# Optimization experiments

Measured on AMD Instinct MI355X. Metric: run time of the kernel, lower is better.

## Reference

```python
import jax, jax.numpy as jnp
import numpy as np

LN_EPS = 1e-5

def _ln(x, g, b):
    m = x.mean(-1, keepdims=True)
    v = ((x - m) ** 2).mean(-1, keepdims=True)
    return (x - m) * jax.lax.rsqrt(v + LN_EPS) * g + b

def setup_inputs() -> dict:
    key = jax.random.key(0)
    B, Q, K, H, NH, L = 4, 32, 8192, 1024, 16, 128
    ks = jax.random.split(key, 10)
    def p(k, shape):
        return jax.random.normal(k, shape, jnp.float32) * 0.02
    return {
        "question_emb": jax.random.normal(ks[0], (B, Q, H), jnp.float32),
        "context_emb": jax.random.normal(ks[1], (B, K, H), jnp.float32),
        "Wq_l": p(ks[2], (H, H)), "bq_l": jnp.zeros((H,), jnp.float32),
        "Wk_l": p(ks[3], (H, H)), "bk_l": jnp.zeros((H,), jnp.float32),
        "Wq_g": p(ks[4], (H, H)), "bq_g": jnp.zeros((H,), jnp.float32),
        "Wk_g": p(ks[5], (H, H)), "bk_g": jnp.zeros((H,), jnp.float32),
        "ln_g": jnp.ones((H,), jnp.float32), "ln_b": jnp.zeros((H,), jnp.float32),
        "gp_W1": p(ks[6], (2 * H, H)), "gp_b1": jnp.zeros((H,), jnp.float32),
        "gp_W2": p(ks[7], (H, 1)), "gp_b2": jnp.zeros((1,), jnp.float32),
        "num_heads": NH,
        "chunk_len": L,
    }

def reference(question_emb, context_emb, Wq_l, bq_l, Wk_l, bk_l,
              Wq_g, bq_g, Wk_g, bk_g, ln_g, ln_b,
              gp_W1, gp_b1, gp_W2, gp_b2, num_heads, chunk_len):
    B, Qn, H = question_emb.shape
    K = context_emb.shape[1]
    nh, L = num_heads, chunk_len
    d = H // nh
    J = K // L
    scale = 1.0 / np.sqrt(d)

    # ---- Global scorer: one cross-attn over all K, then per-chunk mean pooling ----
    qh = (question_emb @ Wq_g + bq_g).reshape(B, Qn, nh, d).transpose(0, 2, 1, 3)   # [B,nh,Q,d]
    kh = (context_emb @ Wk_g + bk_g).reshape(B, K, nh, d).transpose(0, 2, 1, 3)     # [B,nh,K,d]
    wg = jax.nn.softmax(jnp.einsum('bhqd,bhkd->bhqk', qh, kh) * scale, axis=-1)     # [B,nh,Q,K]
    attn = wg.mean(axis=(1, 2))                                                     # [B,K]
    global_scores = jax.nn.softmax(attn.reshape(B, J, L).mean(-1), axis=-1)         # [B,J]

    # ---- Local scorer: per-chunk cross-attn (batched over chunks), max-over-keys pooling ----
    qh_l = (question_emb @ Wq_l + bq_l).reshape(B, Qn, nh, d).transpose(0, 2, 1, 3)  # [B,nh,Q,d]
    kh_l = (context_emb @ Wk_l + bk_l).reshape(B, J, L, nh, d).transpose(0, 1, 3, 2, 4)  # [B,J,nh,L,d]
    s_l = jnp.einsum('bhqd,bjhld->bjhql', qh_l, kh_l) * scale                        # [B,J,nh,Q,L]
    w_l = jax.nn.softmax(s_l, axis=-1)
    local_scores = jax.nn.softmax(w_l.max(-1).mean(axis=(2, 3)), axis=-1)            # [B,J]

    # ---- Router: LN'd mean-pool vecs -> gate MLP -> fuse -> softmax ----
    q_vec = _ln(question_emb.mean(1), ln_g, ln_b)                                    # [B,H]
    c_vec = _ln(context_emb.reshape(B, J, L, H).mean(2), ln_g, ln_b)                 # [B,J,H]
    g_in = jnp.concatenate([jnp.broadcast_to(q_vec[:, None, :], (B, J, H)), c_vec], -1)
    h1 = jax.nn.gelu(g_in @ gp_W1 + gp_b1, approximate=False)
    gate = jax.nn.sigmoid(h1 @ gp_W2 + gp_b2)[..., 0]                                # [B,J]
    fused = gate * local_scores + (1.0 - gate) * global_scores
    final_scores = jax.nn.softmax(fused, axis=-1)                                    # [B,J]
    global_gate = final_scores.mean(-1).reshape(B, 1, 1)
    return final_scores, local_scores, global_scores, global_gate
```

## Files before the change

### kernel.cpp

```cpp
#include <hip/hip_runtime.h>
#include <math.h>

#define B_    4
#define QN    32
#define KN    8192
#define HDIM  1024
#define NHD   16
#define DH    64
#define LCH   128
#define JCH   64

typedef float f32x4 __attribute__((ext_vector_type(4)));
typedef short s16x8 __attribute__((ext_vector_type(8)));
typedef unsigned short u16;

__device__ __forceinline__ u16 f2bf(float f) {
  unsigned u = __float_as_uint(f);
  u += 0x7fffu + ((u >> 16) & 1u);
  return (u16)(u >> 16);
}

__device__ __forceinline__ void llds16(const void* g, void* l) {
  __builtin_amdgcn_global_load_lds((const __attribute__((address_space(1))) unsigned int*)g,
                                   (__attribute__((address_space(3))) unsigned int*)l,
                                   16, 0, 0);
}

__device__ __forceinline__ void gemm64_direct(const float* __restrict__ A, const float* __restrict__ Bm,
                                              float* __restrict__ C, int m0, int n0, char* smem) {
  float (*As)[17] = (float(*)[17])smem;
  float (*Bs)[64] = (float(*)[64])(smem + 4352);
  int t = threadIdx.x;
  int tm = t >> 4, tn = t & 15;
  int ra = t >> 2, ka = (t & 3) * 4;
  int kb = t >> 4, nb = (t & 15) * 4;
  float c[4][4];
#pragma unroll
  for (int i = 0; i < 4; ++i)
#pragma unroll
    for (int j = 0; j < 4; ++j) c[i][j] = 0.f;
  for (int kk = 0; kk < HDIM; kk += 16) {
    float4 va = *(const float4*)(A + (size_t)(m0 + ra) * HDIM + kk + ka);
    float4 vb = *(const float4*)(Bm + (size_t)(kk + kb) * HDIM + n0 + nb);
    As[ra][ka] = va.x; As[ra][ka + 1] = va.y; As[ra][ka + 2] = va.z; As[ra][ka + 3] = va.w;
    *(float4*)&Bs[kb][nb] = vb;
    __syncthreads();
#pragma unroll
    for (int kq = 0; kq < 16; ++kq) {
      float a0 = As[tm * 4 + 0][kq], a1 = As[tm * 4 + 1][kq];
      float a2 = As[tm * 4 + 2][kq], a3 = As[tm * 4 + 3][kq];
      float b0 = Bs[kq][tn * 4 + 0], b1 = Bs[kq][tn * 4 + 1];
      float b2 = Bs[kq][tn * 4 + 2], b3 = Bs[kq][tn * 4 + 3];
      c[0][0] += a0 * b0; c[0][1] += a0 * b1; c[0][2] += a0 * b2; c[0][3] += a0 * b3;
      c[1][0] += a1 * b0; c[1][1] += a1 * b1; c[1][2] += a1 * b2; c[1][3] += a1 * b3;
      c[2][0] += a2 * b0; c[2][1] += a2 * b1; c[2][2] += a2 * b2; c[2][3] += a2 * b3;
      c[3][0] += a3 * b0; c[3][1] += a3 * b1; c[3][2] += a3 * b2; c[3][3] += a3 * b3;
    }
    __syncthreads();
  }
#pragma unroll
  for (int i = 0; i < 4; ++i)
#pragma unroll
    for (int j = 0; j < 4; ++j)
      C[(size_t)(m0 + tm * 4 + i) * HDIM + n0 + tn * 4 + j] = c[i][j];
}

__global__ __launch_bounds__(256) void k_phaseA(const float* __restrict__ ctx, u16* __restrict__ ctxb,
                                                const float* __restrict__ g, const float* __restrict__ lb,
                                                float* __restrict__ cvec,
                                                const float* __restrict__ question,
                                                const float* __restrict__ Wq_g, const float* __restrict__ Wq_l,
                                                float* __restrict__ qh, float* __restrict__ qvec,
                                                float* __restrict__ qpart) {
  __shared__ __align__(16) char smem[8448];
  int blk = blockIdx.x, t = threadIdx.x;
  if (blk < 256) {
    int bj = blk;
    const float* p = ctx + (size_t)bj * LCH * HDIM + t * 4;
    u16* op = ctxb + (size_t)bj * LCH * HDIM + t * 4;
    float a0 = 0, a1 = 0, a2 = 0, a3 = 0;
    for (int r = 0; r < LCH; ++r) {
      float4 v = *(const float4*)(p + (size_t)r * HDIM);
      ushort4 o;
      o.x = f2bf(v.x); o.y = f2bf(v.y); o.z = f2bf(v.z); o.w = f2bf(v.w);
      *(ushort4*)(op + (size_t)r * HDIM) = o;
      a0 += v.x; a1 += v.y; a2 += v.z; a3 += v.w;
    }
    const float sc = 1.0f / LCH;
    a0 *= sc; a1 *= sc; a2 *= sc; a3 *= sc;
    float s = a0 + a1 + a2 + a3;
    float ss = a0 * a0 + a1 * a1 + a2 * a2 + a3 * a3;
#pragma unroll
    for (int o = 1; o < 64; o <<= 1) { s += __shfl_xor(s, o, 64); ss += __shfl_xor(ss, o, 64); }
    float* sm = (float*)smem; float* sq = sm + 4;
    int wid = t >> 6, lane = t & 63;
    if (lane == 0) { sm[wid] = s; sq[wid] = ss; }
    __syncthreads();
    float S = sm[0] + sm[1] + sm[2] + sm[3], SS = sq[0] + sq[1] + sq[2] + sq[3];
    float mu = S / HDIM;
    float inv = rsqrtf(SS / HDIM - mu * mu + 1e-5f);
    int c = t * 4;
    float4 o;
    o.x = (a0 - mu) * inv * g[c + 0] + lb[c + 0];
    o.y = (a1 - mu) * inv * g[c + 1] + lb[c + 1];
    o.z = (a2 - mu) * inv * g[c + 2] + lb[c + 2];
    o.w = (a3 - mu) * inv * g[c + 3] + lb[c + 3];
    *(float4*)&cvec[(size_t)bj * HDIM + c] = o;
  } else if (blk < 320) {
    int id = blk - 256;
    int s2 = id >> 5, mt = (id >> 4) & 1, ntile = id & 15;
    gemm64_direct(question, s2 ? Wq_l : Wq_g, qh + (size_t)s2 * 131072, mt * 64, ntile * 64, smem);
  } else if (blk < 324) {
    int b = blk - 320;
    const float* p = question + (size_t)b * QN * HDIM + t * 4;
    float a0 = 0, a1 = 0, a2 = 0, a3 = 0;
    for (int r = 0; r < QN; ++r) {
      float4 v = *(const float4*)(p + (size_t)r * HDIM);
      a0 += v.x; a1 += v.y; a2 += v.z; a3 += v.w;
    }
    const float sc = 1.0f / QN;
    a0 *= sc; a1 *= sc; a2 *= sc; a3 *= sc;
    float s = a0 + a1 + a2 + a3;
    float ss = a0 * a0 + a1 * a1 + a2 * a2 + a3 * a3;
#pragma unroll
    for (int o = 1; o < 64; o <<= 1) { s += __shfl_xor(s, o, 64); ss += __shfl_xor(ss, o, 64); }
    float* sm = (float*)smem; float* sq = sm + 4;
    int wid = t >> 6, lane = t & 63;
    if (lane == 0) { sm[wid] = s; sq[wid] = ss; }
    __syncthreads();
    float S = sm[0] + sm[1] + sm[2] + sm[3], SS = sq[0] + sq[1] + sq[2] + sq[3];
    float mu = S / HDIM;
    float inv = rsqrtf(SS / HDIM - mu * mu + 1e-5f);
    int c = t * 4;
    float4 o;
    o.x = (a0 - mu) * inv * g[c + 0] + lb[c + 0];
    o.y = (a1 - mu) * inv * g[c + 1] + lb[c + 1];
    o.z = (a2 - mu) * inv * g[c + 2] + lb[c + 2];
    o.w = (a3 - mu) * inv * g[c + 3] + lb[c + 3];
    *(float4*)&qvec[(size_t)b * HDIM + c] = o;
  } else {
    float4 z = make_float4(0.f, 0.f, 0.f, 0.f);
#pragma unroll
    for (int i = 0; i < 4; ++i) ((float4*)qpart)[t * 4 + i] = z;
  }
}

__global__ __launch_bounds__(256) void k_phaseB(const float* __restrict__ qh,
                                                const float* __restrict__ Wk_g, const float* __restrict__ Wk_l,
                                                const float* __restrict__ bq_g, const float* __restrict__ bq_l,
                                                u16* __restrict__ Ab,
                                                const float* __restrict__ bk_g, const float* __restrict__ bk_l,
                                                float* __restrict__ sbias,
                                                const float* __restrict__ qvec, const float* __restrict__ W1,
                                                float* __restrict__ qpart,
                                                const float* __restrict__ cvec, float* __restrict__ h1) {
  __shared__ __align__(16) char smem[8448];
  int blk = blockIdx.x, t = threadIdx.x;
  if (blk < 512) {
    int ct = blk & 3, slot = (blk >> 2) & 31, b = blk >> 7;
    int s2 = slot >> 4, h = slot & 15;
    const float* qhp = qh + (size_t)(s2 * 4 + b) * QN * HDIM;
    const float* Wk = s2 ? Wk_l : Wk_g;
    const float* bq = s2 ? bq_l : bq_g;
    float (*qs)[DH] = (float(*)[DH])smem;
    {
      int q = t >> 3, doff = (t & 7) * 8;
      const float4* src = (const float4*)(qhp + (size_t)q * HDIM + h * DH + doff);
      float4 b0 = *(const float4*)(bq + h * DH + doff);
      float4 b1 = *(const float4*)(bq + h * DH + doff + 4);
      float4 v0 = src[0], v1 = src[1];
      qs[q][doff + 0] = v0.x + b0.x; qs[q][doff + 1] = v0.y + b0.y;
      qs[q][doff + 2] = v0.z + b0.z; qs[q][doff + 3] = v0.w + b0.w;
      qs[q][doff + 4] = v1.x + b1.x; qs[q][doff + 5] = v1.y + b1.y;
      qs[q][doff + 6] = v1.z + b1.z; qs[q][doff + 7] = v1.w + b1.w;
    }
    __syncthreads();
    int c = ct * 256 + t;
    float w[DH];
    const float* wr = Wk + (size_t)c * HDIM + h * DH;
#pragma unroll
    for (int d = 0; d < DH; d += 4) {
      float4 v = *(const float4*)(wr + d);
      w[d] = v.x; w[d + 1] = v.y; w[d + 2] = v.z; w[d + 3] = v.w;
    }
    u16* outp = Ab + ((size_t)b * HDIM + s2 * 512 + h * QN) * HDIM + c;
    for (int q = 0; q < QN; ++q) {
      float acc = 0.f;
#pragma unroll
      for (int d = 0; d < DH; ++d) acc += qs[q][d] * w[d];
      outp[(size_t)q * HDIM] = f2bf(acc * 0.125f);
    }
  } else if (blk < 528) {
    int i = (blk - 512) * 256 + t;
    int b = i >> 10, n = i & (HDIM - 1);
    int s2 = n >> 9, hq = n & 511, h = hq >> 5, q = hq & 31;
    const float* qr = qh + ((size_t)(s2 * 4 + b) * QN + q) * HDIM + h * DH;
    const float* bk = (s2 ? bk_l : bk_g) + h * DH;
    const float* bq = (s2 ? bq_l : bq_g) + h * DH;
    float acc = 0.f;
#pragma unroll
    for (int d = 0; d < DH; ++d) acc += (qr[d] + bq[d]) * bk[d];
    sbias[i] = acc * 0.125f;
  } else if (blk < 784) {
    int id = blk - 528;
    int nt = id & 3, b = (id >> 2) & 3, ks = id >> 4;
    int n = nt * 256 + t;
    const float* qv = qvec + (size_t)b * HDIM + ks * 64;
    const float* wp = W1 + (size_t)ks * 64 * HDIM + n;
    float acc = 0.f;
#pragma unroll 8
    for (int c = 0; c < 64; ++c) acc += qv[c] * wp[(size_t)c * HDIM];
    atomicAdd(&qpart[(size_t)b * HDIM + n], acc);
  } else {
    int id = blk - 784;
    int mt = id >> 4, ntile = id & 15;
    gemm64_direct(cvec, W1 + 1048576, h1, mt * 64, ntile * 64, smem);
  }
}

__global__ __launch_bounds__(512, 2) void k_scores(const u16* __restrict__ ctxb, const u16* __restrict__ Ab,
                                                   const float* __restrict__ sbias,
                                                   float* __restrict__ mglob, float* __restrict__ zglob,
                                                   float* __restrict__ locinv) {
  __shared__ u16 lds[65536];
  u16* A0 = lds;           u16* B0 = lds + 16384;
  u16* A1 = lds + 32768;   u16* B1 = lds + 49152;
  int bid = blockIdx.x;
  int work = (bid & 7) * 64 + (bid >> 3);
  int b = work >> 7, rem = work & 127, rt = rem >> 2, nt = rem & 3;
  int t = threadIdx.x, wid = t >> 6, lane = t & 63;
  int wm = wid >> 2, wn = wid & 3;
  int lrow = lane & 15, lkg = lane >> 4;

  const u16* ctx0 = ctxb + ((size_t)b * KN + rt * 256) * HDIM;
  const u16* Afp  = Ab + ((size_t)b * HDIM + nt * 256) * HDIM;

  int grow = wid * 8 + (lane >> 3);
  int gslot = (lane & 7) ^ (lane >> 3);
  const u16* gA[4]; const u16* gB[4]; int dof[4];
#pragma unroll
  for (int s = 0; s < 4; ++s) {
    gA[s] = ctx0 + (size_t)(s * 64 + grow) * HDIM + gslot * 8;
    gB[s] = Afp + (size_t)(s * 64 + grow) * HDIM + gslot * 8;
    dof[s] = s * 4096 + wid * 512;
  }

  int rowA = (wm * 128 + lrow) * 64;
  int rowB = (wn * 64 + lrow) * 64;
  int p8[2];
#pragma unroll
  for (int ks = 0; ks < 2; ++ks) p8[ks] = ((ks * 4 + lkg) ^ (lane & 7)) * 8;

  f32x4 acc[8][4];
#pragma unroll
  for (int mi = 0; mi < 8; ++mi)
#pragma unroll
    for (int ni = 0; ni < 4; ++ni) acc[mi][ni] = 0.f;

#define STAGE(AT, BT, KT) { \
  _Pragma("unroll") for (int s = 0; s < 4; ++s) { \
    llds16(gA[s] + (KT) * 64, (AT) + dof[s]); \
    llds16(gB[s] + (KT) * 64, (BT) + dof[s]); } }

#define COMPUTE(AT, BT) { \
  _Pragma("unroll") for (int ks = 0; ks < 2; ++ks) { \
    const u16* pA = (AT) + rowA + p8[ks]; \
    const u16* pB = (BT) + rowB + p8[ks]; \
    s16x8 av[8], bv[4]; \
    _Pragma("unroll") for (int mi = 0; mi < 8; ++mi) av[mi] = *(const s16x8*)(pA + mi * 1024); \
    _Pragma("unroll") for (int ni = 0; ni < 4; ++ni) bv[ni] = *(const s16x8*)(pB + ni * 1024); \
    _Pragma("unroll") for (int mi = 0; mi < 8; ++mi) \
    _Pragma("unroll") for (int ni = 0; ni < 4; ++ni) \
      acc[mi][ni] = __builtin_amdgcn_mfma_f32_16x16x32_bf16(av[mi], bv[ni], acc[mi][ni], 0, 0, 0); } }

#define SYNCN(N) { asm volatile("s_waitcnt vmcnt(" #N ")" ::: "memory"); \
                   __builtin_amdgcn_s_barrier(); \
                   __builtin_amdgcn_sched_barrier(0); }

#define SUB(KT, CA, CB, SA, SB, FULL) { \
  if (FULL) { STAGE(SA, SB, (KT) + 1); } \
  if (FULL) { SYNCN(8) } else { SYNCN(0) } \
  __builtin_amdgcn_s_setprio(1); \
  COMPUTE(CA, CB); \
  __builtin_amdgcn_s_setprio(0); \
  __builtin_amdgcn_s_barrier(); }

  STAGE(A0, B0, 0);
  SUB(0,  A0, B0, A1, B1, 1)
  SUB(1,  A1, B1, A0, B0, 1)
  SUB(2,  A0, B0, A1, B1, 1)
  SUB(3,  A1, B1, A0, B0, 1)
  SUB(4,  A0, B0, A1, B1, 1)
  SUB(5,  A1, B1, A0, B0, 1)
  SUB(6,  A0, B0, A1, B1, 1)
  SUB(7,  A1, B1, A0, B0, 1)
  SUB(8,  A0, B0, A1, B1, 1)
  SUB(9,  A1, B1, A0, B0, 1)
  SUB(10, A0, B0, A1, B1, 1)
  SUB(11, A1, B1, A0, B0, 1)
  SUB(12, A0, B0, A1, B1, 1)
  SUB(13, A1, B1, A0, B0, 1)
  SUB(14, A0, B0, A1, B1, 1)
  SUB(15, A1, B1, A0, B0, 0)
#undef STAGE
#undef COMPUTE
#undef SYNCN
#undef SUB

  int jc = rt * 2 + wm;
  float sb[4];
#pragma unroll
  for (int ni = 0; ni < 4; ++ni)
    sb[ni] = sbias[b * HDIM + nt * 256 + wn * 64 + ni * 16 + lrow];
#pragma unroll
  for (int ni = 0; ni < 4; ++ni) {
    float m = -1e30f;
#pragma unroll
    for (int mi = 0; mi < 8; ++mi)
#pragma unroll
      for (int r = 0; r < 4; ++r) m = fmaxf(m, acc[mi][ni][r]);
    m += sb[ni];
    m = fmaxf(m, __shfl_xor(m, 16, 64));
    m = fmaxf(m, __shfl_xor(m, 32, 64));
    float z = 0.f;
#pragma unroll
    for (int mi = 0; mi < 8; ++mi)
#pragma unroll
      for (int r = 0; r < 4; ++r) z += __expf(acc[mi][ni][r] + sb[ni] - m);
    z += __shfl_xor(z, 16, 64);
    z += __shfl_xor(z, 32, 64);
    if (lane < 16) {
      int n = nt * 256 + wn * 64 + ni * 16 + lane;
      if (n < 512) {
        size_t o = ((size_t)b * 512 + n) * JCH + jc;
        mglob[o] = m; zglob[o] = z;
      } else {
        locinv[((size_t)b * JCH + jc) * 512 + (n - 512)] = 1.0f / z;
      }
    }
  }
}

__global__ __launch_bounds__(256) void k_hq(const float* __restrict__ mglob, const float* __restrict__ zglob,
                                            float* __restrict__ Mh, float* __restrict__ Zr) {
  int id = blockIdx.x * 256 + threadIdx.x;
  int b = id >> 9, hq = id & 511;
  const float* mg = mglob + ((size_t)b * 512 + hq) * JCH;
  const float* zg = zglob + ((size_t)b * 512 + hq) * JCH;
  float m = -1e30f;
  for (int j = 0; j < JCH; ++j) m = fmaxf(m, mg[j]);
  float z = 0.f;
  for (int j = 0; j < JCH; ++j) z += zg[j] * __expf(mg[j] - m);
  Mh[id] = m;
  Zr[id] = 1.0f / z;
}

__global__ __launch_bounds__(256) void k_chunk(const float* __restrict__ mglob, const float* __restrict__ zglob,
                                               const float* __restrict__ locinv,
                                               const float* __restrict__ Mh, const float* __restrict__ Zr,
                                               const float* __restrict__ h1, const float* __restrict__ qpart,
                                               const float* __restrict__ b1, const float* __restrict__ W2,
                                               float* __restrict__ abuf, float* __restrict__ lbuf,
                                               float* __restrict__ gbuf) {
  int bj = blockIdx.x, t = threadIdx.x;
  int b = bj >> 6, j = bj & 63;
  const float* mg = mglob + (size_t)b * 512 * JCH + j;
  const float* zg = zglob + (size_t)b * 512 * JCH + j;
  const float* lp = locinv + (size_t)bj * 512;
  const float* Mb = Mh + (size_t)b * 512;
  const float* Zb = Zr + (size_t)b * 512;
  float a = 0.f, l = 0.f, gsum = 0.f;
  for (int hq = t; hq < 512; hq += 256) {
    a += zg[(size_t)hq * JCH] * __expf(mg[(size_t)hq * JCH] - Mb[hq]) * Zb[hq];
    l += lp[hq];
  }
  const float* hp = h1 + (size_t)bj * HDIM;
  const float* qp = qpart + (size_t)b * HDIM;
  for (int n = t; n < HDIM; n += 256) {
    float x = hp[n] + qp[n] + b1[n];
    x = x * 0.5f * (1.0f + erff(x * 0.70710678118654752f));
    gsum += x * W2[n];
  }
#pragma unroll
  for (int o = 1; o < 64; o <<= 1) {
    a += __shfl_xor(a, o, 64); l += __shfl_xor(l, o, 64); gsum += __shfl_xor(gsum, o, 64);
  }
  __shared__ float ra[4], rl[4], rg[4];
  int wid = t >> 6, lane = t & 63;
  if (lane == 0) { ra[wid] = a; rl[wid] = l; rg[wid] = gsum; }
  __syncthreads();
  if (t == 0) {
    abuf[bj] = (ra[0] + ra[1] + ra[2] + ra[3]) * (1.0f / 65536.0f);
    lbuf[bj] = (rl[0] + rl[1] + rl[2] + rl[3]) * (1.0f / 512.0f);
    gbuf[bj] = rg[0] + rg[1] + rg[2] + rg[3];
  }
}

__global__ __launch_bounds__(64) void k_final(const float* __restrict__ abuf, const float* __restrict__ lbuf,
                                              const float* __restrict__ gbuf, const float* __restrict__ b2,
                                              float* __restrict__ out) {
  int b = blockIdx.x, t = threadIdx.x;
  float a = abuf[b * 64 + t];
  float l = lbuf[b * 64 + t];
  float gt = gbuf[b * 64 + t] + b2[0];
  gt = 1.0f / (1.0f + __expf(-gt));
  float am = a, lm = l;
#pragma unroll
  for (int o = 1; o < 64; o <<= 1) { am = fmaxf(am, __shfl_xor(am, o, 64)); lm = fmaxf(lm, __shfl_xor(lm, o, 64)); }
  float ae = __expf(a - am), le = __expf(l - lm);
  float as_ = ae, ls_ = le;
#pragma unroll
  for (int o = 1; o < 64; o <<= 1) { as_ += __shfl_xor(as_, o, 64); ls_ += __shfl_xor(ls_, o, 64); }
  float gs = ae / as_, ls = le / ls_;
  float fu = gt * ls + (1.0f - gt) * gs;
  float fm = fu;
#pragma unroll
  for (int o = 1; o < 64; o <<= 1) fm = fmaxf(fm, __shfl_xor(fm, o, 64));
  float fe = __expf(fu - fm);
  float fs_ = fe;
#pragma unroll
  for (int o = 1; o < 64; o <<= 1) fs_ += __shfl_xor(fs_, o, 64);
  float fv = fe / fs_;
  out[b * 64 + t] = fv;
  out[256 + b * 64 + t] = ls;
  out[512 + b * 64 + t] = gs;
  float tot = fv;
#pragma unroll
  for (int o = 1; o < 64; o <<= 1) tot += __shfl_xor(tot, o, 64);
  if (t == 0) out[768 + b] = tot * (1.0f / 64.0f);
}

extern "C" void kernel_launch(void* const* d_in, const int* in_sizes, int n_in,
                              void* d_out, int out_size, void* d_ws, size_t ws_size,
                              hipStream_t stream) {
  const float* question = (const float*)d_in[0];
  const float* context  = (const float*)d_in[1];
  const float* Wq_l = (const float*)d_in[2];
  const float* bq_l = (const float*)d_in[3];
  const float* Wk_l = (const float*)d_in[4];
  const float* bk_l = (const float*)d_in[5];
  const float* Wq_g = (const float*)d_in[6];
  const float* bq_g = (const float*)d_in[7];
  const float* Wk_g = (const float*)d_in[8];
  const float* bk_g = (const float*)d_in[9];
  const float* ln_g = (const float*)d_in[10];
  const float* ln_b = (const float*)d_in[11];
  const float* W1   = (const float*)d_in[12];
  const float* b1   = (const float*)d_in[13];
  const float* W2   = (const float*)d_in[14];
  const float* b2   = (const float*)d_in[15];

  char* ws = (char*)d_ws;
  u16*   ctxb   = (u16*)(ws + 0);
  u16*   Ab     = (u16*)(ws + 67108864);
  float* qh     = (float*)(ws + 75497472);
  float* sbias  = (float*)(ws + 76546048);
  float* mglob  = (float*)(ws + 76562432);
  float* zglob  = (float*)(ws + 77086720);
  float* locinv = (float*)(ws + 77611008);
  float* qvec   = (float*)(ws + 78135296);
  float* cvec   = (float*)(ws + 78151680);
  float* qpart  = (float*)(ws + 79200256);
  float* h1     = (float*)(ws + 79216640);
  float* Mh     = (float*)(ws + 80265216);
  float* Zr     = (float*)(ws + 80273408);
  float* abuf   = (float*)(ws + 80281600);
  float* lbuf   = (float*)(ws + 80282624);
  float* gbuf   = (float*)(ws + 80283648);

  hipLaunchKernelGGL(k_phaseA, dim3(325), dim3(256), 0, stream,
                     context, ctxb, ln_g, ln_b, cvec, question, Wq_g, Wq_l, qh, qvec, qpart);
  hipLaunchKernelGGL(k_phaseB, dim3(848), dim3(256), 0, stream,
                     qh, Wk_g, Wk_l, bq_g, bq_l, Ab, bk_g, bk_l, sbias, qvec, W1, qpart, cvec, h1);
  hipLaunchKernelGGL(k_scores, dim3(512), dim3(512), 0, stream, ctxb, Ab, sbias, mglob, zglob, locinv);
  hipLaunchKernelGGL(k_hq, dim3(8), dim3(256), 0, stream, mglob, zglob, Mh, Zr);
  hipLaunchKernelGGL(k_chunk, dim3(256), dim3(256), 0, stream, mglob, zglob, locinv, Mh, Zr, h1, qpart, b1, W2, abuf, lbuf, gbuf);
  hipLaunchKernelGGL(k_final, dim3(4), dim3(64), 0, stream, abuf, lbuf, gbuf, b2, (float*)d_out);
}
```

Before: 230.4 us.

## Split context conversion across row segments and defer LN/gate GEMM to later kernels

Result: slower. 245.8 us (+6.7%).

```diff
diff --git a/kernel.cpp b/kernel.cpp
--- a/kernel.cpp
+++ b/kernel.cpp
@@ -65,53 +65,36 @@
       C[(size_t)(m0 + tm * 4 + i) * HDIM + n0 + tn * 4 + j] = c[i][j];
 }
 
-__global__ __launch_bounds__(256) void k_phaseA(const float* __restrict__ ctx, u16* __restrict__ ctxb,
-                                                const float* __restrict__ g, const float* __restrict__ lb,
-                                                float* __restrict__ cvec,
-                                                const float* __restrict__ question,
-                                                const float* __restrict__ Wq_g, const float* __restrict__ Wq_l,
-                                                float* __restrict__ qh, float* __restrict__ qvec,
-                                                float* __restrict__ qpart) {
+__global__ __launch_bounds__(256) void k_cvt(const float* __restrict__ ctx, u16* __restrict__ ctxb,
+                                             float* __restrict__ csum4,
+                                             const float* __restrict__ question,
+                                             const float* __restrict__ Wq_g, const float* __restrict__ Wq_l,
+                                             float* __restrict__ qh,
+                                             const float* __restrict__ g, const float* __restrict__ lb,
+                                             float* __restrict__ qvec, float* __restrict__ qpart) {
   __shared__ __align__(16) char smem[8448];
   int blk = blockIdx.x, t = threadIdx.x;
-  if (blk < 256) {
-    int bj = blk;
-    const float* p = ctx + (size_t)bj * LCH * HDIM + t * 4;
-    u16* op = ctxb + (size_t)bj * LCH * HDIM + t * 4;
+  if (blk < 1024) {
+    int bj = blk >> 2, seg = blk & 3;
+    const float* p = ctx + ((size_t)bj * LCH + seg * 32) * HDIM + t * 4;
+    u16* op = ctxb + ((size_t)bj * LCH + seg * 32) * HDIM + t * 4;
     float a0 = 0, a1 = 0, a2 = 0, a3 = 0;
-    for (int r = 0; r < LCH; ++r) {
+#pragma unroll 8
+    for (int r = 0; r < 32; ++r) {
       float4 v = *(const float4*)(p + (size_t)r * HDIM);
       ushort4 o;
       o.x = f2bf(v.x); o.y = f2bf(v.y); o.z = f2bf(v.z); o.w = f2bf(v.w);
       *(ushort4*)(op + (size_t)r * HDIM) = o;
       a0 += v.x; a1 += v.y; a2 += v.z; a3 += v.w;
     }
-    const float sc = 1.0f / LCH;
-    a0 *= sc; a1 *= sc; a2 *= sc; a3 *= sc;
-    float s = a0 + a1 + a2 + a3;
-    float ss = a0 * a0 + a1 * a1 + a2 * a2 + a3 * a3;
-#pragma unroll
-    for (int o = 1; o < 64; o <<= 1) { s += __shfl_xor(s, o, 64); ss += __shfl_xor(ss, o, 64); }
-    float* sm = (float*)smem; float* sq = sm + 4;
-    int wid = t >> 6, lane = t & 63;
-    if (lane == 0) { sm[wid] = s; sq[wid] = ss; }
-    __syncthreads();
-    float S = sm[0] + sm[1] + sm[2] + sm[3], SS = sq[0] + sq[1] + sq[2] + sq[3];
-    float mu = S / HDIM;
-    float inv = rsqrtf(SS / HDIM - mu * mu + 1e-5f);
-    int c = t * 4;
-    float4 o;
-    o.x = (a0 - mu) * inv * g[c + 0] + lb[c + 0];
-    o.y = (a1 - mu) * inv * g[c + 1] + lb[c + 1];
-    o.z = (a2 - mu) * inv * g[c + 2] + lb[c + 2];
-    o.w = (a3 - mu) * inv * g[c + 3] + lb[c + 3];
-    *(float4*)&cvec[(size_t)bj * HDIM + c] = o;
-  } else if (blk < 320) {
-    int id = blk - 256;
+    float4 s4 = make_float4(a0, a1, a2, a3);
+    *(float4*)&csum4[((size_t)bj * 4 + seg) * HDIM + t * 4] = s4;
+  } else if (blk < 1088) {
+    int id = blk - 1024;
     int s2 = id >> 5, mt = (id >> 4) & 1, ntile = id & 15;
     gemm64_direct(question, s2 ? Wq_l : Wq_g, qh + (size_t)s2 * 131072, mt * 64, ntile * 64, smem);
-  } else if (blk < 324) {
-    int b = blk - 320;
+  } else if (blk < 1092) {
+    int b = blk - 1088;
     const float* p = question + (size_t)b * QN * HDIM + t * 4;
     float a0 = 0, a1 = 0, a2 = 0, a3 = 0;
     for (int r = 0; r < QN; ++r) {
@@ -145,15 +128,17 @@
   }
 }
 
-__global__ __launch_bounds__(256) void k_phaseB(const float* __restrict__ qh,
-                                                const float* __restrict__ Wk_g, const float* __restrict__ Wk_l,
-                                                const float* __restrict__ bq_g, const float* __restrict__ bq_l,
-                                                u16* __restrict__ Ab,
-                                                const float* __restrict__ bk_g, const float* __restrict__ bk_l,
-                                                float* __restrict__ sbias,
-                                                const float* __restrict__ qvec, const float* __restrict__ W1,
-                                                float* __restrict__ qpart,
-                                                const float* __restrict__ cvec, float* __restrict__ h1) {
+__global__ __launch_bounds__(256) void k_mid(const float* __restrict__ qh,
+                                             const float* __restrict__ Wk_g, const float* __restrict__ Wk_l,
+                                             const float* __restrict__ bq_g, const float* __restrict__ bq_l,
+                                             u16* __restrict__ Ab,
+                                             const float* __restrict__ bk_g, const float* __restrict__ bk_l,
+                                             float* __restrict__ sbias,
+                                             const float* __restrict__ qvec, const float* __restrict__ W1,
+                                             float* __restrict__ qpart,
+                                             const float* __restrict__ csum4,
+                                             const float* __restrict__ g, const float* __restrict__ lb,
+                                             float* __restrict__ cvec) {
   __shared__ __align__(16) char smem[8448];
   int blk = blockIdx.x, t = threadIdx.x;
   if (blk < 512) {
@@ -212,9 +197,35 @@
     for (int c = 0; c < 64; ++c) acc += qv[c] * wp[(size_t)c * HDIM];
     atomicAdd(&qpart[(size_t)b * HDIM + n], acc);
   } else {
-    int id = blk - 784;
-    int mt = id >> 4, ntile = id & 15;
-    gemm64_direct(cvec, W1 + 1048576, h1, mt * 64, ntile * 64, smem);
+    int bj = blk - 784;
+    const float* cs = csum4 + (size_t)bj * 4 * HDIM + t * 4;
+    float4 v0 = *(const float4*)(cs);
+    float4 v1 = *(const float4*)(cs + HDIM);
+    float4 v2 = *(const float4*)(cs + 2 * HDIM);
+    float4 v3 = *(const float4*)(cs + 3 * HDIM);
+    const float sc = 1.0f / LCH;
+    float a0 = (v0.x + v1.x + v2.x + v3.x) * sc;
+    float a1 = (v0.y + v1.y + v2.y + v3.y) * sc;
+    float a2 = (v0.z + v1.z + v2.z + v3.z) * sc;
+    float a3 = (v0.w + v1.w + v2.w + v3.w) * sc;
+    float s = a0 + a1 + a2 + a3;
+    float ss = a0 * a0 + a1 * a1 + a2 * a2 + a3 * a3;
+#pragma unroll
+    for (int o = 1; o < 64; o <<= 1) { s += __shfl_xor(s, o, 64); ss += __shfl_xor(ss, o, 64); }
+    float* sm = (float*)smem; float* sq = sm + 4;
+    int wid = t >> 6, lane = t & 63;
+    if (lane == 0) { sm[wid] = s; sq[wid] = ss; }
+    __syncthreads();
+    float S = sm[0] + sm[1] + sm[2] + sm[3], SS = sq[0] + sq[1] + sq[2] + sq[3];
+    float mu = S / HDIM;
+    float inv = rsqrtf(SS / HDIM - mu * mu + 1e-5f);
+    int c = t * 4;
+    float4 o;
+    o.x = (a0 - mu) * inv * g[c + 0] + lb[c + 0];
+    o.y = (a1 - mu) * inv * g[c + 1] + lb[c + 1];
+    o.z = (a2 - mu) * inv * g[c + 2] + lb[c + 2];
+    o.w = (a3 - mu) * inv * g[c + 3] + lb[c + 3];
+    *(float4*)&cvec[(size_t)bj * HDIM + c] = o;
   }
 }
 
@@ -341,18 +352,27 @@
   }
 }
 
-__global__ __launch_bounds__(256) void k_hq(const float* __restrict__ mglob, const float* __restrict__ zglob,
-                                            float* __restrict__ Mh, float* __restrict__ Zr) {
-  int id = blockIdx.x * 256 + threadIdx.x;
-  int b = id >> 9, hq = id & 511;
-  const float* mg = mglob + ((size_t)b * 512 + hq) * JCH;
-  const float* zg = zglob + ((size_t)b * 512 + hq) * JCH;
-  float m = -1e30f;
-  for (int j = 0; j < JCH; ++j) m = fmaxf(m, mg[j]);
-  float z = 0.f;
-  for (int j = 0; j < JCH; ++j) z += zg[j] * __expf(mg[j] - m);
-  Mh[id] = m;
-  Zr[id] = 1.0f / z;
+__global__ __launch_bounds__(256) void k_post(const float* __restrict__ cvec, const float* __restrict__ W1,
+                                              float* __restrict__ h1,
+                                              const float* __restrict__ mglob, const float* __restrict__ zglob,
+                                              float* __restrict__ Mh, float* __restrict__ Zr) {
+  __shared__ __align__(16) char smem[8448];
+  int blk = blockIdx.x, t = threadIdx.x;
+  if (blk < 64) {
+    int mt = blk >> 4, ntile = blk & 15;
+    gemm64_direct(cvec, W1 + 1048576, h1, mt * 64, ntile * 64, smem);
+  } else {
+    int id = (blk - 64) * 256 + t;
+    int b = id >> 9, hq = id & 511;
+    const float* mg = mglob + ((size_t)b * 512 + hq) * JCH;
+    const float* zg = zglob + ((size_t)b * 512 + hq) * JCH;
+    float m = -1e30f;
+    for (int j = 0; j < JCH; ++j) m = fmaxf(m, mg[j]);
+    float z = 0.f;
+    for (int j = 0; j < JCH; ++j) z += zg[j] * __expf(mg[j] - m);
+    Mh[id] = m;
+    Zr[id] = 1.0f / z;
+  }
 }
 
 __global__ __launch_bounds__(256) void k_chunk(const float* __restrict__ mglob, const float* __restrict__ zglob,
@@ -467,13 +487,15 @@
   float* abuf   = (float*)(ws + 80281600);
   float* lbuf   = (float*)(ws + 80282624);
   float* gbuf   = (float*)(ws + 80283648);
-
-  hipLaunchKernelGGL(k_phaseA, dim3(325), dim3(256), 0, stream,
-                     context, ctxb, ln_g, ln_b, cvec, question, Wq_g, Wq_l, qh, qvec, qpart);
-  hipLaunchKernelGGL(k_phaseB, dim3(848), dim3(256), 0, stream,
-                     qh, Wk_g, Wk_l, bq_g, bq_l, Ab, bk_g, bk_l, sbias, qvec, W1, qpart, cvec, h1);
+  float* csum4  = (float*)(ws + 80284672);
+
+  hipLaunchKernelGGL(k_cvt, dim3(1093), dim3(256), 0, stream,
+                     context, ctxb, csum4, question, Wq_g, Wq_l, qh, ln_g, ln_b, qvec, qpart);
+  hipLaunchKernelGGL(k_mid, dim3(1040), dim3(256), 0, stream,
+                     qh, Wk_g, Wk_l, bq_g, bq_l, Ab, bk_g, bk_l, sbias, qvec, W1, qpart,
+                     csum4, ln_g, ln_b, cvec);
   hipLaunchKernelGGL(k_scores, dim3(512), dim3(512), 0, stream, ctxb, Ab, sbias, mglob, zglob, locinv);
-  hipLaunchKernelGGL(k_hq, dim3(8), dim3(256), 0, stream, mglob, zglob, Mh, Zr);
+  hipLaunchKernelGGL(k_post, dim3(72), dim3(256), 0, stream, cvec, W1, h1, mglob, zglob, Mh, Zr);
   hipLaunchKernelGGL(k_chunk, dim3(256), dim3(256), 0, stream, mglob, zglob, locinv, Mh, Zr, h1, qpart, b1, W2, abuf, lbuf, gbuf);
   hipLaunchKernelGGL(k_final, dim3(4), dim3(64), 0, stream, abuf, lbuf, gbuf, b2, (float*)d_out);
 }
```
